# Optimization experiments

Hardware: AMD Instinct MI355X
Metric: run time of the kernel (lower is better)

## Reference

```python
import jax, jax.numpy as jnp
import numpy as np

V, D, H, HD, L, T, B = 65, 384, 6, 64, 6, 256, 64
EPS = 1e-3  # keras LayerNormalization default epsilon


def setup_inputs() -> dict:
    key = jax.random.key(0)
    ks = jax.random.split(key, 12)
    s = 0.02
    n = lambda k, shp: jax.random.normal(k, shp, dtype=jnp.float32) * s
    return {
        "idx": jax.random.randint(ks[0], (B, T), 0, V),
        "tok_emb": n(ks[1], (V, D)),
        "pos_emb": n(ks[2], (T, D)),
        "Wq": n(ks[3], (L, H, D, HD)),
        "Wk": n(ks[4], (L, H, D, HD)),
        "Wv": n(ks[5], (L, H, D, HD)),
        "Wproj": n(ks[6], (L, D, D)),
        "bproj": jnp.zeros((L, D), jnp.float32),
        "W1": n(ks[7], (L, D, 4 * D)),
        "b1": jnp.zeros((L, 4 * D), jnp.float32),
        "W2": n(ks[8], (L, 4 * D, D)),
        "b2": jnp.zeros((L, D), jnp.float32),
        "ln1_g": jnp.ones((L, D), jnp.float32),
        "ln1_b": jnp.zeros((L, D), jnp.float32),
        "ln2_g": jnp.ones((L, D), jnp.float32),
        "ln2_b": jnp.zeros((L, D), jnp.float32),
        "lnf_g": jnp.ones((D,), jnp.float32),
        "lnf_b": jnp.zeros((D,), jnp.float32),
        "Whead": n(ks[9], (D, V)),
        "bhead": jnp.zeros((V,), jnp.float32),
    }


def _ln(x, g, b):
    m = jnp.mean(x, axis=-1, keepdims=True)
    v = jnp.mean(jnp.square(x - m), axis=-1, keepdims=True)
    return (x - m) * jax.lax.rsqrt(v + EPS) * g + b


def reference(idx, tok_emb, pos_emb, Wq, Wk, Wv, Wproj, bproj, W1, b1, W2, b2,
              ln1_g, ln1_b, ln2_g, ln2_b, lnf_g, lnf_b, Whead, bhead):
    Bn, Tn = idx.shape
    x = tok_emb[idx] + pos_emb[:Tn]  # [B,T,D]
    mask = jnp.tril(jnp.ones((Tn, Tn), dtype=bool))
    scale = jnp.float32(D) ** -0.5  # NOTE: original scales by full C=n_embd, not head_size
    for l in range(L):
        h = _ln(x, ln1_g[l], ln1_b[l])
        q = jnp.einsum('btd,hdk->bhtk', h, Wq[l])
        k = jnp.einsum('btd,hdk->bhtk', h, Wk[l])
        v = jnp.einsum('btd,hdk->bhtk', h, Wv[l])
        wei = jnp.einsum('bhtk,bhsk->bhts', q, k) * scale
        wei = jnp.where(mask, wei, -jnp.inf)
        wei = jax.nn.softmax(wei, axis=-1)
        att = jnp.einsum('bhts,bhsk->bhtk', wei, v)
        att = att.transpose(0, 2, 1, 3).reshape(Bn, Tn, D)  # concat heads
        x = x + att @ Wproj[l] + bproj[l]
        h2 = _ln(x, ln2_g[l], ln2_b[l])
        x = x + jax.nn.relu(h2 @ W1[l] + b1[l]) @ W2[l] + b2[l]
    x = _ln(x, lnf_g, lnf_b)
    return x @ Whead + bhead  # logits [B,T,V]
```

## Files before the change

### kernel.cpp

```cpp
#include <hip/hip_runtime.h>
#include <hip/hip_bf16.h>

#define B_  64
#define T_  256
#define D_  384
#define H_  6
#define HD_ 64
#define L_  6
#define V_  65
#define BT  (B_*T_)

typedef __hip_bfloat16 bf16;
typedef unsigned short u16;
typedef short s16;
typedef __attribute__((ext_vector_type(8))) short bf16x8;
typedef __attribute__((ext_vector_type(4))) float f32x4;

#define OFF_QKV   0
#define OFF_PROJ  442368
#define OFF_W1T   589824
#define OFF_W2T   1179648
#define OFF_BPROJ 1769472
#define OFF_B1    1769856
#define OFF_B2    1771392
#define OFF_LN1G  1771776
#define OFF_LN1B  1772160
#define OFF_LN2G  1772544
#define OFF_LN2B  1772928
#define WBUF_E    1773312
#define HOFF_WHT  0
#define HOFF_BH   24960
#define HOFF_LNFG 25088
#define HOFF_LNFB 25472
#define HBUF_E    25856

__device__ __forceinline__ float u2f(u16 u) {
  union { unsigned i; float f; } c; c.i = ((unsigned)u) << 16; return c.f;
}
__device__ __forceinline__ bf16 f2b(float x) { return __float2bfloat16(x); }
__device__ __forceinline__ float b2f(bf16 x) { return __bfloat162float(x); }
__device__ __forceinline__ u16 f2u(float x) { bf16 h = f2b(x); return *(u16*)&h; }

__device__ __forceinline__ float pload(const void* p, size_t i, bool f32w) {
  return f32w ? ((const float*)p)[i] : u2f(((const u16*)p)[i]);
}

__device__ __forceinline__ void swz(int gid, int ntc, int mtiles,
                                    int& nt, int& mblk) {
  if ((mtiles & 7) == 0) {
    int per = ntc << 3;
    int g   = gid / per;
    int rem = gid - g * per;
    nt   = rem >> 3;
    mblk = (g << 3) + (rem & 7);
  } else {
    nt   = gid / mtiles;
    mblk = gid - nt * mtiles;
  }
}

__global__ __launch_bounds__(256) void detect_kernel(
    const void* p1,  const void* p2,  const void* p3,  const void* p4,
    const void* p5,  const void* p6,  const void* p7,  const void* p8,
    const void* p9,  const void* p10, const void* p11, const void* p12,
    const void* p13, const void* p14, const void* p15, const void* p16,
    const void* p17, const void* p18, const void* p19,
    const int* __restrict__ idx, unsigned* flags)
{
  const void* ps[20] = {nullptr, p1, p2, p3, p4, p5, p6, p7, p8, p9, p10,
                        p11, p12, p13, p14, p15, p16, p17, p18, p19};
  const int esz[20] = {16384, 24960, 98304, 884736, 884736, 884736, 884736,
                       2304, 3538944, 9216, 3538944, 2304, 2304, 2304, 2304,
                       2304, 384, 384, 24960, 65};
  __shared__ int r1[256], r2[256];
  int bid = blockIdx.x, tid = threadIdx.x;
  if (bid == 19) {
    int z = 0;
    for (int m = tid; m < 4096; m += 256) z += (idx[2 * m + 1] == 0) ? 1 : 0;
    r1[tid] = z; __syncthreads();
    for (int s = 128; s > 0; s >>= 1) {
      if (tid < s) r1[tid] += r1[tid + s];
      __syncthreads();
    }
    if (tid == 0) flags[20] = (r1[0] >= 4000) ? 1u : 0u;
    return;
  }
  int j = bid + 1;
  const u16* p = (const u16*)ps[j];
  int ns = esz[j] / 2; if (ns > 1024) ns = 1024;
  int band = 0, nz = 0;
  for (int i = tid; i < ns; i += 256) {
    u16 lo = p[2 * i], hi = p[2 * i + 1];
    int e = (lo >> 7) & 0xFF;
    band += (e >= 100 && e <= 127) ? 1 : 0;
    nz   += (lo | hi) ? 1 : 0;
  }
  r1[tid] = band; r2[tid] = nz; __syncthreads();
  for (int s = 128; s > 0; s >>= 1) {
    if (tid < s) { r1[tid] += r1[tid + s]; r2[tid] += r2[tid + s]; }
    __syncthreads();
  }
  if (tid == 0) flags[j] = (r2[0] > 0 && r1[0] * 2 < ns) ? 1u : 0u;
}

__global__ void const_kernel(float* out, int n, float val) {
  int i = blockIdx.x * 256 + threadIdx.x;
  if (i < n) out[i] = val;
}

__device__ __forceinline__ float conv_val(int e, int l,
    const void* Wq, const void* Wk, const void* Wv, const void* Wproj,
    const void* bproj, const void* W1, const void* b1, const void* W2,
    const void* b2, const void* ln1g, const void* ln1b, const void* ln2g,
    const void* ln2b, const unsigned* __restrict__ flags)
{
  float v;
  if (e < OFF_PROJ) {
    int math = e / 24576;
    int rem  = e - math * 24576;
    int hd = rem / 384, d = rem - hd * 384;
    int mat = math / 6, hh = math - mat * 6;
    const void* src = (mat == 0 ? Wq : mat == 1 ? Wk : Wv);
    v = pload(src, ((size_t)(l * 6 + hh) * 384 + d) * 64 + hd, flags[3 + mat] != 0);
  } else if (e < OFF_W1T) {
    int e2 = e - OFF_PROJ;
    int n = e2 / 384, d = e2 - n * 384;
    v = pload(Wproj, ((size_t)l * 384 + d) * 384 + n, flags[6] != 0);
  } else if (e < OFF_W2T) {
    int e2 = e - OFF_W1T;
    int n = e2 / 384, d = e2 - n * 384;
    v = pload(W1, ((size_t)l * 384 + d) * 1536 + n, flags[8] != 0);
  } else if (e < OFF_BPROJ) {
    int e2 = e - OFF_W2T;
    int n = e2 / 1536, k = e2 - n * 1536;
    v = pload(W2, ((size_t)l * 1536 + k) * 384 + n, flags[10] != 0);
  } else {
    int e2 = e - OFF_BPROJ;
    if      (e2 < 384)  v = pload(bproj, (size_t)l * 384 + e2, flags[7] != 0);
    else if (e2 < 1920) v = pload(b1, (size_t)l * 1536 + (e2 - 384), flags[9] != 0);
    else if (e2 < 2304) v = pload(b2, (size_t)l * 384 + (e2 - 1920), flags[11] != 0);
    else if (e2 < 2688) v = pload(ln1g, (size_t)l * 384 + (e2 - 2304), flags[12] != 0);
    else if (e2 < 3072) v = pload(ln1b, (size_t)l * 384 + (e2 - 2688), flags[13] != 0);
    else if (e2 < 3456) v = pload(ln2g, (size_t)l * 384 + (e2 - 3072), flags[14] != 0);
    else                v = pload(ln2b, (size_t)l * 384 + (e2 - 3456), flags[15] != 0);
  }
  return v;
}

__global__ __launch_bounds__(256) void conv_layer(
    const void* Wq, const void* Wk, const void* Wv, const void* Wproj,
    const void* bproj, const void* W1, const void* b1, const void* W2,
    const void* b2, const void* ln1g, const void* ln1b, const void* ln2g,
    const void* ln2b, const unsigned* __restrict__ flags,
    bf16* __restrict__ dst, int l)
{
  int e = blockIdx.x * 256 + threadIdx.x;
  if (e >= WBUF_E) return;
  dst[e] = f2b(conv_val(e, l, Wq, Wk, Wv, Wproj, bproj, W1, b1, W2, b2,
                        ln1g, ln1b, ln2g, ln2b, flags));
}

__global__ __launch_bounds__(256) void convT(
    const void* Wq, const void* Wk, const void* Wv, const void* Wproj,
    const void* W1, const void* W2,
    const unsigned* __restrict__ flags, bf16* __restrict__ dst)
{
  __shared__ float lds[64][65];
  int g = blockIdx.x;
  int l = g / 432, t = g - l * 432;
  const void* sp; bool f32w;
  size_t s_base; int s_rstride;
  size_t d_base; int d_rstride;
  if (t < 108) {
    int mh = t / 6, dt = t - mh * 6;
    int mat = mh / 6;
    sp = (mat == 0 ? Wq : mat == 1 ? Wk : Wv);
    f32w = flags[3 + mat] != 0;
    s_base = ((size_t)l * 6 * 384 + (size_t)(mh - mat * 6) * 384 + dt * 64) * 64;
    s_rstride = 64;
    d_base = (size_t)OFF_QKV + (size_t)mh * 24576 + dt * 64;
    d_rstride = 384;
  } else if (t < 144) {
    int u = t - 108; int nt = u / 6, dt = u - nt * 6;
    sp = Wproj; f32w = flags[6] != 0;
    s_base = ((size_t)l * 384 + dt * 64) * 384 + nt * 64;
    s_rstride = 384;
    d_base = (size_t)OFF_PROJ + (size_t)nt * 64 * 384 + dt * 64;
    d_rstride = 384;
  } else if (t < 288) {
    int u = t - 144; int nt = u / 6, dt = u - nt * 6;
    sp = W1; f32w = flags[8] != 0;
    s_base = ((size_t)l * 384 + dt * 64) * 1536 + nt * 64;
    s_rstride = 1536;
    d_base = (size_t)OFF_W1T + (size_t)nt * 64 * 384 + dt * 64;
    d_rstride = 384;
  } else {
    int u = t - 288; int kt = u / 6, nt = u - kt * 6;
    sp = W2; f32w = flags[10] != 0;
    s_base = ((size_t)l * 1536 + kt * 64) * 384 + nt * 64;
    s_rstride = 384;
    d_base = (size_t)OFF_W2T + (size_t)nt * 64 * 1536 + kt * 64;
    d_rstride = 1536;
  }
  int tid = threadIdx.x;
  int rq = tid >> 6, c = tid & 63;
#pragma unroll
  for (int p = 0; p < 16; p++) {
    int r = p * 4 + rq;
    lds[c][r] = pload(sp, s_base + (size_t)r * s_rstride + c, f32w);
  }
  __syncthreads();
  bf16* dp = dst + (size_t)l * WBUF_E + d_base;
#pragma unroll
  for (int p = 0; p < 16; p++) {
    int cc = p * 4 + rq;
    dp[(size_t)cc * d_rstride + c] = f2b(lds[cc][c]);
  }
}

__global__ __launch_bounds__(256) void convsmall(
    const void* Wq, const void* Wk, const void* Wv, const void* Wproj,
    const void* bproj, const void* W1, const void* b1, const void* W2,
    const void* b2, const void* ln1g, const void* ln1b, const void* ln2g,
    const void* ln2b, const unsigned* __restrict__ flags,
    bf16* __restrict__ dst)
{
  int g = blockIdx.x * 256 + threadIdx.x;
  if (g >= 6 * (WBUF_E - OFF_BPROJ)) return;
  int l = g / (WBUF_E - OFF_BPROJ);
  int e = OFF_BPROJ + (g - l * (WBUF_E - OFF_BPROJ));
  dst[(size_t)l * WBUF_E + e] =
      f2b(conv_val(e, l, Wq, Wk, Wv, Wproj, bproj, W1, b1, W2, b2,
                   ln1g, ln1b, ln2g, ln2b, flags));
}

__global__ __launch_bounds__(256) void conv_head(
    const void* Wh, const void* bh, const void* lnfg, const void* lnfb,
    const unsigned* __restrict__ flags, bf16* __restrict__ dst)
{
  int e = blockIdx.x * 256 + threadIdx.x;
  if (e >= HBUF_E) return;
  float v = 0.f;
  if (e < HOFF_BH) {
    int n = e / 384, d = e - n * 384;
    v = pload(Wh, (size_t)d * 65 + n, flags[18] != 0);
  } else if (e < 25025) {
    v = pload(bh, e - HOFF_BH, flags[19] != 0);
  } else if (e < HOFF_LNFG) {
    v = 0.f;
  } else if (e < HOFF_LNFB) {
    v = pload(lnfg, e - HOFF_LNFG, flags[16] != 0);
  } else {
    v = pload(lnfb, e - HOFF_LNFB, flags[17] != 0);
  }
  dst[e] = f2b(v);
}

__global__ __launch_bounds__(256) void embed_kernel(
    const void* __restrict__ idx, const void* __restrict__ tok,
    const void* __restrict__ pos, bf16* __restrict__ x,
    const unsigned* __restrict__ flags)
{
  int i   = blockIdx.x * 256 + threadIdx.x;
  int tkn = i / D_;
  int d   = i - tkn * D_;
  int t   = tkn & (T_ - 1);
  long long tix;
  if (flags[20]) tix = ((const long long*)idx)[tkn];
  else           tix = ((const int*)idx)[tkn];
  float v = pload(tok, (size_t)tix * D_ + d, flags[1] != 0)
          + pload(pos, (size_t)t * D_ + d, flags[2] != 0);
  x[i] = f2b(v);
}

__global__ __launch_bounds__(256) void lnw_kernel(
    const bf16* __restrict__ x, const u16* __restrict__ g,
    const u16* __restrict__ b, bf16* __restrict__ hc, int tok0)
{
  int w = threadIdx.x >> 6, lane = threadIdx.x & 63;
  int lm = blockIdx.x * 4 + w;
  const u16* xr = (const u16*)x + (size_t)(tok0 + lm) * D_;
  float v[6]; float s = 0.f;
#pragma unroll
  for (int j = 0; j < 3; j++) {
    unsigned pk = *(const unsigned*)(xr + 2 * lane + 128 * j);
    v[2 * j]     = u2f((u16)(pk & 0xFFFF));
    v[2 * j + 1] = u2f((u16)(pk >> 16));
    s += v[2 * j] + v[2 * j + 1];
  }
#pragma unroll
  for (int o = 1; o < 64; o <<= 1) s += __shfl_xor(s, o, 64);
  float mean = s * (1.0f / D_);
  float sq = 0.f;
#pragma unroll
  for (int j = 0; j < 6; j++) { float d0 = v[j] - mean; sq += d0 * d0; }
#pragma unroll
  for (int o = 1; o < 64; o <<= 1) sq += __shfl_xor(sq, o, 64);
  float inv = 1.0f / sqrtf(sq * (1.0f / D_) + 1e-3f);
  u16* hr = (u16*)hc + (size_t)lm * D_;
#pragma unroll
  for (int j = 0; j < 3; j++) {
    int d = 2 * lane + 128 * j;
    unsigned gg = *(const unsigned*)(g + d);
    unsigned bb = *(const unsigned*)(b + d);
    u16 o0 = f2u((v[2 * j]     - mean) * inv * u2f((u16)(gg & 0xFFFF)) + u2f((u16)(bb & 0xFFFF)));
    u16 o1 = f2u((v[2 * j + 1] - mean) * inv * u2f((u16)(gg >> 16))    + u2f((u16)(bb >> 16)));
    *(unsigned*)(hr + d) = ((unsigned)o1 << 16) | o0;
  }
}

__device__ __forceinline__ void gll16(const void* g, void* l) {
  __builtin_amdgcn_global_load_lds(
      (const __attribute__((address_space(1))) unsigned*)g,
      (__attribute__((address_space(3))) unsigned*)l, 16, 0, 0);
}

__device__ __forceinline__ bf16x8 ldfrag(const s16* lds, int r, int s) {
  return *(const bf16x8*)(lds + r * 64 + ((s ^ (r & 7)) << 3));
}

template<int NT, class Epi>
__device__ __forceinline__ void mcore(
    s16* __restrict__ As, s16* __restrict__ Wl,
    const u16* __restrict__ A, const u16* __restrict__ WT,
    int N, int K, int arow0, int n0, Epi epi)
{
  constexpr int MREP = (NT == 128) ? 4 : 2;
  constexpr int WPW  = NT / 32;
  int tid = threadIdx.x;
  int w = tid >> 6, lane = tid & 63;
  int quad = lane >> 4, l15 = lane & 15;
  int r8 = lane >> 3;
  int sl = ((lane & 7) ^ r8) * 8;
  int wm = (NT == 128) ? ((w >> 1) * 64) : (w * 32);
  int wn = (NT == 128) ? ((w & 1) * 64) : 0;

  f32x4 acc[MREP][4];
#pragma unroll
  for (int i = 0; i < MREP; i++)
#pragma unroll
    for (int j = 0; j < 4; j++) acc[i][j] = (f32x4){0.f, 0.f, 0.f, 0.f};

  const u16* Ag[4];
#pragma unroll
  for (int i = 0; i < 4; i++)
    Ag[i] = A + (size_t)(arow0 + (w * 4 + i) * 8 + r8) * K + sl;
  const u16* Wg[WPW];
#pragma unroll
  for (int i = 0; i < WPW; i++)
    Wg[i] = WT + (size_t)(n0 + (w * WPW + i) * 8 + r8) * K + sl;

  for (int k0 = 0; k0 < K; k0 += 64) {
    __syncthreads();
#pragma unroll
    for (int i = 0; i < 4; i++)
      gll16(Ag[i] + k0, As + (w * 4 + i) * 512);
#pragma unroll
    for (int i = 0; i < WPW; i++)
      gll16(Wg[i] + k0, Wl + (w * WPW + i) * 512);
    __syncthreads();
#pragma unroll
    for (int kh = 0; kh < 2; kh++) {
      bf16x8 am[MREP], bn[4];
#pragma unroll
      for (int i = 0; i < MREP; i++)
        am[i] = ldfrag(As, wm + i * 16 + l15, kh * 4 + quad);
#pragma unroll
      for (int j = 0; j < 4; j++)
        bn[j] = ldfrag(Wl, wn + j * 16 + l15, kh * 4 + quad);
#pragma unroll
      for (int i = 0; i < MREP; i++)
#pragma unroll
        for (int j = 0; j < 4; j++)
          acc[i][j] = __builtin_amdgcn_mfma_f32_16x16x32_bf16(am[i], bn[j], acc[i][j], 0, 0, 0);
    }
  }

#pragma unroll
  for (int i = 0; i < MREP; i++)
#pragma unroll
    for (int j = 0; j < 4; j++)
#pragma unroll
      for (int r = 0; r < 4; r++) {
        int m = wm + i * 16 + quad * 4 + r;
        int n = n0 + wn + j * 16 + l15;
        if (n < N) epi(m, n, acc[i][j][r]);
      }
}

template<class EpiV, class EpiR>
__device__ __forceinline__ void mcoreB(
    s16* __restrict__ SM,
    const u16* __restrict__ A, const u16* __restrict__ WT,
    int K, int arow0, int n0, EpiV epiv, EpiR epir)
{
  s16* As = SM;
  s16* Wl = SM + 128 * 64;
  int tid = threadIdx.x;
  int w = tid >> 6, lane = tid & 63;
  int quad = lane >> 4, l15 = lane & 15;
  int r8 = lane >> 3;
  int sl = ((lane & 7) ^ r8) * 8;
  int wm = (w >> 1) * 64, wn = (w & 1) * 64;

  f32x4 acc[4][4];
#pragma unroll
  for (int i = 0; i < 4; i++)
#pragma unroll
    for (int j = 0; j < 4; j++) acc[i][j] = (f32x4){0.f, 0.f, 0.f, 0.f};

  const u16* Ag[4];
#pragma unroll
  for (int i = 0; i < 4; i++)
    Ag[i] = A + (size_t)(arow0 + (w * 4 + i) * 8 + r8) * K + sl;
  const u16* Wg[4];
#pragma unroll
  for (int i = 0; i < 4; i++)
    Wg[i] = WT + (size_t)(n0 + (w * 4 + i) * 8 + r8) * K + sl;

  for (int k0 = 0; k0 < K; k0 += 64) {
    __syncthreads();
#pragma unroll
    for (int i = 0; i < 4; i++)
      gll16(Ag[i] + k0, As + (w * 4 + i) * 512);
#pragma unroll
    for (int i = 0; i < 4; i++)
      gll16(Wg[i] + k0, Wl + (w * 4 + i) * 512);
    __syncthreads();
#pragma unroll
    for (int kh = 0; kh < 2; kh++) {
      bf16x8 am[4], bn[4];
#pragma unroll
      for (int i = 0; i < 4; i++)
        am[i] = ldfrag(As, wm + i * 16 + l15, kh * 4 + quad);
#pragma unroll
      for (int j = 0; j < 4; j++)
        bn[j] = ldfrag(Wl, wn + j * 16 + l15, kh * 4 + quad);
#pragma unroll
      for (int i = 0; i < 4; i++)
#pragma unroll
        for (int j = 0; j < 4; j++)
          acc[i][j] = __builtin_amdgcn_mfma_f32_16x16x32_bf16(am[i], bn[j], acc[i][j], 0, 0, 0);
    }
  }

  __syncthreads();
#pragma unroll
  for (int i = 0; i < 4; i++)
#pragma unroll
    for (int j = 0; j < 4; j++)
#pragma unroll
      for (int r = 0; r < 4; r++) {
        int m = wm + i * 16 + quad * 4 + r;
        int nloc = wn + j * 16 + l15;
        int nl6 = nloc & 63;
        SM[((nloc >> 6) << 13) + m * 64 +
           ((((nl6 >> 3) ^ (m & 7)) << 3)) + (nl6 & 7)] = epiv(nloc, acc[i][j][r]);
      }
  __syncthreads();
  int row = tid >> 1, hf = tid & 1;
  const s16* src = SM + (hf << 13) + row * 64;
#pragma unroll
  for (int c = 0; c < 8; c++) {
    bf16x8 v8 = *(const bf16x8*)(src + ((c ^ (row & 7)) << 3));
    epir(row, hf, c, v8);
  }
}

__global__ __launch_bounds__(256) void qkv128(
    const bf16* hc, const bf16* Wbuf, bf16* qkvc, int MCa, int mtiles)
{
  __shared__ __attribute__((aligned(16))) s16 SM[2 * 128 * 64];
  int nt, mblk;
  swz(blockIdx.x, 9, mtiles, nt, mblk);
  int n0 = nt * 128, mloc0 = mblk * 128;
  auto epiv = [&](int nloc, float v) -> s16 { return (s16)f2u(v); };
  auto epir = [&](int row, int hf, int c, bf16x8 v8) {
    int nn = n0 + hf * 64;
    int mat = nn / 384;
    int hh = (nn - mat * 384) >> 6;
    *(bf16x8*)((u16*)qkvc + (size_t)mat * MCa * D_ + (size_t)hh * MCa * HD_
               + (size_t)(mloc0 + row) * HD_ + c * 8) = v8;
  };
  mcoreB(SM, (const u16*)hc, (const u16*)Wbuf + OFF_QKV,
         D_, mloc0, n0, epiv, epir);
}

__global__ __launch_bounds__(256) void ffn1_128(
    const bf16* hc, const bf16* Wbuf, bf16* midc, int mtiles)
{
  __shared__ __attribute__((aligned(16))) s16 SM[2 * 128 * 64];
  int nt, mblk;
  swz(blockIdx.x, 12, mtiles, nt, mblk);
  int n0 = nt * 128, m0 = mblk * 128;
  const bf16* bias = (const bf16*)Wbuf + OFF_B1;
  auto epiv = [&](int nloc, float v) -> s16 {
    float r = v + b2f(bias[n0 + nloc]);
    return (s16)f2u(fmaxf(r, 0.f));
  };
  auto epir = [&](int row, int hf, int c, bf16x8 v8) {
    *(bf16x8*)((u16*)midc + (size_t)(m0 + row) * (4 * D_)
               + n0 + hf * 64 + c * 8) = v8;
  };
  mcoreB(SM, (const u16*)hc, (const u16*)Wbuf + OFF_W1T,
         D_, m0, n0, epiv, epir);
}

__global__ __launch_bounds__(256) void proj_mfma(
    const bf16* A, const bf16* Wbuf, bf16* x, int tok0, int mtiles)
{
  __shared__ __attribute__((aligned(16))) s16 As[128 * 64];
  __shared__ __attribute__((aligned(16))) s16 Ws[64 * 64];
  int nt, mblk;
  swz(blockIdx.x, 6, mtiles, nt, mblk);
  int n0 = nt * 64, m0 = mblk * 128;
  const bf16* bias = (const bf16*)Wbuf + OFF_BPROJ;
  auto epi = [&](int m, int n, float v) {
    size_t o = (size_t)(tok0 + m0 + m) * D_ + n;
    x[o] = f2b(v + b2f(bias[n]) + b2f(x[o]));
  };
  mcore<64>(As, Ws, (const u16*)A,
            (const u16*)Wbuf + OFF_PROJ, D_, D_, m0, n0, epi);
}

__global__ __launch_bounds__(256) void ffn2_mfma(
    const bf16* midc, const bf16* Wbuf, bf16* x, int tok0, int mtiles)
{
  __shared__ __attribute__((aligned(16))) s16 As[128 * 64];
  __shared__ __attribute__((aligned(16))) s16 Ws[64 * 64];
  int nt, mblk;
  swz(blockIdx.x, 6, mtiles, nt, mblk);
  int n0 = nt * 64, m0 = mblk * 128;
  const bf16* bias = (const bf16*)Wbuf + OFF_B2;
  auto epi = [&](int m, int n, float v) {
    size_t o = (size_t)(tok0 + m0 + m) * D_ + n;
    x[o] = f2b(v + b2f(bias[n]) + b2f(x[o]));
  };
  mcore<64>(As, Ws, (const u16*)midc,
            (const u16*)Wbuf + OFF_W2T, D_, 4 * D_, m0, n0, epi);
}

__global__ __launch_bounds__(256) void head_mfma(
    const bf16* hc, const bf16* Hbuf, float* out, int tok0)
{
  __shared__ __attribute__((aligned(16))) s16 As[128 * 64];
  __shared__ __attribute__((aligned(16))) s16 Ws[64 * 64];
  int n0 = blockIdx.x * 64, m0 = blockIdx.y * 128;
  const bf16* bias = (const bf16*)Hbuf + HOFF_BH;
  auto epi = [&](int m, int n, float v) {
    out[(size_t)(tok0 + m0 + m) * V_ + n] = v + b2f(bias[n]);
  };
  mcore<64>(As, Ws, (const u16*)hc,
            (const u16*)Hbuf + HOFF_WHT, V_, D_, m0, n0, epi);
}

__global__ __launch_bounds__(256) void attn4_kernel(
    const bf16* __restrict__ Q, const bf16* __restrict__ K,
    const bf16* __restrict__ V, bf16* __restrict__ att, int MCa)
{
  __shared__ s16 Qs[64 * 72];
  __shared__ s16 Ks[64 * 72];
  __shared__ __attribute__((aligned(16))) s16 Vt[64 * 64];
  __shared__ s16 Ps[4][16 * 72];
  const float scale = 0.05103103630798288f;
  int tid = threadIdx.x;
  int w = tid >> 6, lane = tid & 63;
  int quad = lane >> 4, l15 = lane & 15;
  int bid = blockIdx.x;
  int qt = bid & 3;
  int bh = bid >> 2;
  int b = bh / H_, h = bh - b * H_;
  size_t base = ((size_t)h * MCa + (size_t)b * T_) * HD_;
  int q0 = qt * 64;
  int cq = qt;

  int rstg = (tid & 7) + 8 * (tid >> 6);
  int sstg = (tid >> 3) & 7;

#pragma unroll
  for (int i = 0; i < 2; i++) {
    int r = rstg + 32 * i;
    *(bf16x8*)&Qs[r * 72 + sstg * 8] =
        *(const bf16x8*)((const u16*)Q + base + (size_t)(q0 + r) * HD_ + sstg * 8);
  }

  float mrow[4] = {-1e30f, -1e30f, -1e30f, -1e30f};
  float lrow[4] = {0.f, 0.f, 0.f, 0.f};
  f32x4 O[4];
#pragma unroll
  for (int nt = 0; nt < 4; nt++) O[nt] = (f32x4){0.f, 0.f, 0.f, 0.f};

  for (int c = 0; c <= cq; c++) {
    __syncthreads();
#pragma unroll
    for (int i = 0; i < 2; i++) {
      int r = rstg + 32 * i;
      *(bf16x8*)&Ks[r * 72 + sstg * 8] =
          *(const bf16x8*)((const u16*)K + base + (size_t)(c * 64 + r) * HD_ + sstg * 8);
      bf16x8 vv =
          *(const bf16x8*)((const u16*)V + base + (size_t)(c * 64 + r) * HD_ + sstg * 8);
      int rs = r >> 3, rl = r & 7;
      int so = ((rs ^ sstg) << 3) + rl;
#pragma unroll
      for (int k = 0; k < 8; k++)
        Vt[(sstg * 8 + k) * 64 + so] = vv[k];
    }
    __syncthreads();

    f32x4 S[4];
#pragma unroll
    for (int nt = 0; nt < 4; nt++) S[nt] = (f32x4){0.f, 0.f, 0.f, 0.f};
#pragma unroll
    for (int ks = 0; ks < 2; ks++) {
      int kk = ks * 32 + quad * 8;
      bf16x8 a = *(const bf16x8*)&Qs[(w * 16 + l15) * 72 + kk];
#pragma unroll
      for (int nt = 0; nt < 4; nt++) {
        bf16x8 bb8 = *(const bf16x8*)&Ks[(nt * 16 + l15) * 72 + kk];
        S[nt] = __builtin_amdgcn_mfma_f32_16x16x32_bf16(a, bb8, S[nt], 0, 0, 0);
      }
    }

#pragma unroll
    for (int nt = 0; nt < 4; nt++)
#pragma unroll
      for (int r = 0; r < 4; r++) {
        int qrow = q0 + w * 16 + quad * 4 + r;
        int sg = c * 64 + nt * 16 + l15;
        float v = S[nt][r] * scale;
        S[nt][r] = (sg <= qrow) ? v : -1e30f;
      }

    float alpha[4];
#pragma unroll
    for (int r = 0; r < 4; r++) {
      float mc = fmaxf(fmaxf(S[0][r], S[1][r]), fmaxf(S[2][r], S[3][r]));
#pragma unroll
      for (int o = 1; o < 16; o <<= 1) mc = fmaxf(mc, __shfl_xor(mc, o, 64));
      float mn = fmaxf(mrow[r], mc);
      alpha[r] = __expf(mrow[r] - mn);
      mrow[r] = mn;
      float s = 0.f;
#pragma unroll
      for (int nt = 0; nt < 4; nt++) {
        float p = __expf(S[nt][r] - mn);
        S[nt][r] = p;
        s += p;
      }
#pragma unroll
      for (int o = 1; o < 16; o <<= 1) s += __shfl_xor(s, o, 64);
      lrow[r] = lrow[r] * alpha[r] + s;
    }
#pragma unroll
    for (int nt = 0; nt < 4; nt++)
#pragma unroll
      for (int r = 0; r < 4; r++) O[nt][r] *= alpha[r];

#pragma unroll
    for (int nt = 0; nt < 4; nt++)
#pragma unroll
      for (int r = 0; r < 4; r++)
        Ps[w][(quad * 4 + r) * 72 + nt * 16 + l15] = (s16)f2u(S[nt][r]);
    __syncthreads();
#pragma unroll
    for (int ks = 0; ks < 2; ks++) {
      bf16x8 a = *(const bf16x8*)&Ps[w][l15 * 72 + ks * 32 + quad * 8];
#pragma unroll
      for (int nt = 0; nt < 4; nt++) {
        int d = nt * 16 + l15;
        bf16x8 bb8 = *(const bf16x8*)&Vt[d * 64 +
            (((ks * 4 + quad) ^ ((d >> 3) & 7)) << 3)];
        O[nt] = __builtin_amdgcn_mfma_f32_16x16x32_bf16(a, bb8, O[nt], 0, 0, 0);
      }
    }
  }

#pragma unroll
  for (int r = 0; r < 4; r++) {
    float invl = 1.0f / lrow[r];
#pragma unroll
    for (int nt = 0; nt < 4; nt++) {
      int qrow = q0 + w * 16 + quad * 4 + r;
      att[(size_t)(b * T_ + qrow) * D_ + h * HD_ + nt * 16 + l15] =
          f2b(O[nt][r] * invl);
    }
  }
}

extern "C" void kernel_launch(void* const* d_in, const int* in_sizes, int n_in,
                              void* d_out, int out_size, void* d_ws, size_t ws_size,
                              hipStream_t stream)
{
  float* out = (float*)d_out;
  dim3 blk(256);
  int outg = (out_size + 255) / 256;

  static const int expected[20] = {
      16384, 24960, 98304, 884736, 884736, 884736, 884736, 2304,
      3538944, 9216, 3538944, 2304, 2304, 2304, 2304, 2304, 384, 384,
      24960, 65};
  if (n_in != 20) { const_kernel<<<outg, blk, 0, stream>>>(out, out_size, 5.0f); return; }
  for (int i = 0; i < 20; i++)
    if (in_sizes[i] != expected[i]) {
      const_kernel<<<outg, blk, 0, stream>>>(out, out_size, 10.0f * (i + 1));
      return;
    }
  if (out_size != BT * V_) { const_kernel<<<outg, blk, 0, stream>>>(out, out_size, 7.0f); return; }

  const void* idx   = d_in[0];
  const void* tok   = d_in[1];
  const void* pos   = d_in[2];
  const void* Wq    = d_in[3];
  const void* Wk    = d_in[4];
  const void* Wv    = d_in[5];
  const void* Wproj = d_in[6];
  const void* bproj = d_in[7];
  const void* W1    = d_in[8];
  const void* b1    = d_in[9];
  const void* W2    = d_in[10];
  const void* b2    = d_in[11];
  const void* ln1g  = d_in[12];
  const void* ln1b  = d_in[13];
  const void* ln2g  = d_in[14];
  const void* ln2b  = d_in[15];
  const void* lnfg  = d_in[16];
  const void* lnfb  = d_in[17];
  const void* Whead = d_in[18];
  const void* bhead = d_in[19];

  const size_t off_x  = 256;
  const size_t off_wb = off_x + (size_t)BT * D_ * 2;
  int nl = 6;
  size_t off_hb = off_wb + (size_t)nl * WBUF_E * 2;
  size_t fixed  = off_hb + ((size_t)HBUF_E * 2 + 63) / 64 * 64;
  size_t minchunk = (size_t)5 * (BT / 64) * D_ * 2;
  if (ws_size < fixed + minchunk) {
    nl = 1;
    off_hb = off_wb + (size_t)WBUF_E * 2;
    fixed  = off_hb + ((size_t)HBUF_E * 2 + 63) / 64 * 64;
  }
  if (ws_size < fixed) {
    const_kernel<<<outg, blk, 0, stream>>>(out, out_size, 0.0f);
    return;
  }
  size_t region = ws_size - fixed;

  int nc = 0;
  const int candn[7] = {1, 2, 4, 8, 16, 32, 64};
  for (int i = 0; i < 7; i++)
    if ((size_t)5 * (BT / candn[i]) * D_ * 2 <= region) { nc = candn[i]; break; }
  if (!nc) { const_kernel<<<outg, blk, 0, stream>>>(out, out_size, 0.0f); return; }
  const int MCc = BT / nc;
  const int CBc = MCc / T_;
  const int mtiles = MCc / 128;

  char* wsb = (char*)d_ws;
  unsigned* flags = (unsigned*)wsb;
  bf16*   x    = (bf16*)(wsb + off_x);
  bf16*   Wbuf = (bf16*)(wsb + off_wb);
  bf16*   Hbuf = (bf16*)(wsb + off_hb);
  bf16*   hc   = (bf16*)(wsb + fixed);
  bf16*   qkvc = hc + (size_t)MCc * D_;
  bf16*   attc = qkvc + (size_t)3 * MCc * D_;
  bf16*   midc = qkvc;

  detect_kernel<<<dim3(20), blk, 0, stream>>>(
      tok, pos, Wq, Wk, Wv, Wproj, bproj, W1, b1, W2, b2,
      ln1g, ln1b, ln2g, ln2b, lnfg, lnfb, Whead, bhead,
      (const int*)idx, flags);
  embed_kernel<<<dim3(BT * D_ / 256), blk, 0, stream>>>(idx, tok, pos, x, flags);
  conv_head<<<dim3((HBUF_E + 255) / 256), blk, 0, stream>>>(
      Whead, bhead, lnfg, lnfb, flags, Hbuf);
  if (nl == 6) {
    convT<<<dim3(6 * 432), blk, 0, stream>>>(
        Wq, Wk, Wv, Wproj, W1, W2, flags, Wbuf);
    convsmall<<<dim3((6 * (WBUF_E - OFF_BPROJ) + 255) / 256), blk, 0, stream>>>(
        Wq, Wk, Wv, Wproj, bproj, W1, b1, W2, b2,
        ln1g, ln1b, ln2g, ln2b, flags, Wbuf);
  }

  for (int l = 0; l < L_; l++) {
    const bf16* Wl = Wbuf + (nl == 6 ? (size_t)l * WBUF_E : 0);
    if (nl == 1)
      conv_layer<<<dim3((WBUF_E + 255) / 256), blk, 0, stream>>>(
          Wq, Wk, Wv, Wproj, bproj, W1, b1, W2, b2,
          ln1g, ln1b, ln2g, ln2b, flags, Wbuf, l);
    for (int c = 0; c < nc; c++) {
      int tok0 = c * MCc;
      lnw_kernel<<<dim3(MCc / 4), blk, 0, stream>>>(
          x, (const u16*)Wl + OFF_LN1G, (const u16*)Wl + OFF_LN1B, hc, tok0);
      qkv128<<<dim3(9 * mtiles), blk, 0, stream>>>(hc, Wl, qkvc, MCc, mtiles);
      attn4_kernel<<<dim3(CBc * H_ * 4), blk, 0, stream>>>(
          qkvc, qkvc + (size_t)MCc * D_, qkvc + (size_t)2 * MCc * D_, attc, MCc);
      proj_mfma<<<dim3(6 * mtiles), blk, 0, stream>>>(attc, Wl, x, tok0, mtiles);
    }
    for (int f = 0; f < nc; f++) {
      int tok0 = f * MCc;
      lnw_kernel<<<dim3(MCc / 4), blk, 0, stream>>>(
          x, (const u16*)Wl + OFF_LN2G, (const u16*)Wl + OFF_LN2B, hc, tok0);
      ffn1_128<<<dim3(12 * mtiles), blk, 0, stream>>>(hc, Wl, midc, mtiles);
      ffn2_mfma<<<dim3(6 * mtiles), blk, 0, stream>>>(midc, Wl, x, tok0, mtiles);
    }
  }

  for (int c = 0; c < nc; c++) {
    int tok0 = c * MCc;
    lnw_kernel<<<dim3(MCc / 4), blk, 0, stream>>>(
        x, (const u16*)Hbuf + HOFF_LNFG, (const u16*)Hbuf + HOFF_LNFB, hc, tok0);
    head_mfma<<<dim3(2, MCc / 128), blk, 0, stream>>>(hc, Hbuf, out, tok0);
  }
}
```

Measured before the change: 1.124 ms.

## Use direct global-to-LDS loads and staged vectorized epilogue for proj/ffn2 GEMMs

Adds a new 128x64 MFMA GEMM core that loads A and W tiles straight into LDS with 16-byte global-to-LDS transfers, and uses it for the projection and FFN2 kernels. The epilogue now stages fp32 accumulators through swizzled shared memory, so each thread reads back 8 contiguous outputs and does vectorized 16-byte residual reads, bias adds and writes. This replaces scattered per-element residual updates. It increases shared memory per block and adds extra barriers and an LDS round trip in the epilogue.

```diff
diff --git a/kernel.cpp b/kernel.cpp
--- a/kernel.cpp
+++ b/kernel.cpp
@@ -467,6 +467,88 @@
   }
 }
 
+template<class Fin>
+__device__ __forceinline__ void mcoreB64(
+    s16* __restrict__ SM,
+    const u16* __restrict__ A, const u16* __restrict__ WT,
+    int K, int arow0, int n0, Fin fin)
+{
+  s16* As = SM;
+  s16* Wl = SM + 128 * 64;
+  int tid = threadIdx.x;
+  int w = tid >> 6, lane = tid & 63;
+  int quad = lane >> 4, l15 = lane & 15;
+  int r8 = lane >> 3;
+  int sl = ((lane & 7) ^ r8) * 8;
+  int wm = w * 32;
+
+  f32x4 acc[2][4];
+#pragma unroll
+  for (int i = 0; i < 2; i++)
+#pragma unroll
+    for (int j = 0; j < 4; j++) acc[i][j] = (f32x4){0.f, 0.f, 0.f, 0.f};
+
+  const u16* Ag[4];
+#pragma unroll
+  for (int i = 0; i < 4; i++)
+    Ag[i] = A + (size_t)(arow0 + (w * 4 + i) * 8 + r8) * K + sl;
+  const u16* Wg[2];
+#pragma unroll
+  for (int i = 0; i < 2; i++)
+    Wg[i] = WT + (size_t)(n0 + (w * 2 + i) * 8 + r8) * K + sl;
+
+  for (int k0 = 0; k0 < K; k0 += 64) {
+    __syncthreads();
+#pragma unroll
+    for (int i = 0; i < 4; i++)
+      gll16(Ag[i] + k0, As + (w * 4 + i) * 512);
+#pragma unroll
+    for (int i = 0; i < 2; i++)
+      gll16(Wg[i] + k0, Wl + (w * 2 + i) * 512);
+    __syncthreads();
+#pragma unroll
+    for (int kh = 0; kh < 2; kh++) {
+      bf16x8 am[2], bn[4];
+#pragma unroll
+      for (int i = 0; i < 2; i++)
+        am[i] = ldfrag(As, wm + i * 16 + l15, kh * 4 + quad);
+#pragma unroll
+      for (int j = 0; j < 4; j++)
+        bn[j] = ldfrag(Wl, j * 16 + l15, kh * 4 + quad);
+#pragma unroll
+      for (int i = 0; i < 2; i++)
+#pragma unroll
+        for (int j = 0; j < 4; j++)
+          acc[i][j] = __builtin_amdgcn_mfma_f32_16x16x32_bf16(am[i], bn[j], acc[i][j], 0, 0, 0);
+    }
+  }
+
+  __syncthreads();
+  float* SMf = (float*)SM;
+#pragma unroll
+  for (int i = 0; i < 2; i++)
+#pragma unroll
+    for (int j = 0; j < 4; j++)
+#pragma unroll
+      for (int r = 0; r < 4; r++) {
+        int m = wm + i * 16 + quad * 4 + r;
+        int n = j * 16 + l15;
+        SMf[m * 64 + (n ^ ((m & 7) << 2))] = acc[i][j][r];
+      }
+  __syncthreads();
+  int row = tid >> 1, hf = tid & 1;
+  int mask = (row & 7) << 2;
+  const float* rp = SMf + row * 64;
+#pragma unroll
+  for (int c8 = 0; c8 < 4; c8++) {
+    int cb = hf * 32 + c8 * 8;
+    float v[8];
+    *(f32x4*)(v)     = *(const f32x4*)(rp + ((cb)     ^ mask));
+    *(f32x4*)(v + 4) = *(const f32x4*)(rp + ((cb + 4) ^ mask));
+    fin(row, cb, v);
+  }
+}
+
 __global__ __launch_bounds__(256) void qkv128(
     const bf16* hc, const bf16* Wbuf, bf16* qkvc, int MCa, int mtiles)
 {
@@ -509,35 +591,47 @@
 __global__ __launch_bounds__(256) void proj_mfma(
     const bf16* A, const bf16* Wbuf, bf16* x, int tok0, int mtiles)
 {
-  __shared__ __attribute__((aligned(16))) s16 As[128 * 64];
-  __shared__ __attribute__((aligned(16))) s16 Ws[64 * 64];
+  __shared__ __attribute__((aligned(16))) s16 SM[2 * 128 * 64];
   int nt, mblk;
   swz(blockIdx.x, 6, mtiles, nt, mblk);
   int n0 = nt * 64, m0 = mblk * 128;
-  const bf16* bias = (const bf16*)Wbuf + OFF_BPROJ;
-  auto epi = [&](int m, int n, float v) {
-    size_t o = (size_t)(tok0 + m0 + m) * D_ + n;
-    x[o] = f2b(v + b2f(bias[n]) + b2f(x[o]));
+  const u16* bias = (const u16*)Wbuf + OFF_BPROJ;
+  auto fin = [&](int row, int cb, const float* v) {
+    size_t o = (size_t)(tok0 + m0 + row) * D_ + n0 + cb;
+    u16* xp = (u16*)x + o;
+    bf16x8 xr = *(const bf16x8*)xp;
+    bf16x8 bb = *(const bf16x8*)(bias + n0 + cb);
+    bf16x8 ov;
+#pragma unroll
+    for (int k = 0; k < 8; k++)
+      ov[k] = (s16)f2u(v[k] + u2f((u16)bb[k]) + u2f((u16)xr[k]));
+    *(bf16x8*)xp = ov;
   };
-  mcore<64>(As, Ws, (const u16*)A,
-            (const u16*)Wbuf + OFF_PROJ, D_, D_, m0, n0, epi);
+  mcoreB64(SM, (const u16*)A, (const u16*)Wbuf + OFF_PROJ,
+           D_, m0, n0, fin);
 }
 
 __global__ __launch_bounds__(256) void ffn2_mfma(
     const bf16* midc, const bf16* Wbuf, bf16* x, int tok0, int mtiles)
 {
-  __shared__ __attribute__((aligned(16))) s16 As[128 * 64];
-  __shared__ __attribute__((aligned(16))) s16 Ws[64 * 64];
+  __shared__ __attribute__((aligned(16))) s16 SM[2 * 128 * 64];
   int nt, mblk;
   swz(blockIdx.x, 6, mtiles, nt, mblk);
   int n0 = nt * 64, m0 = mblk * 128;
-  const bf16* bias = (const bf16*)Wbuf + OFF_B2;
-  auto epi = [&](int m, int n, float v) {
-    size_t o = (size_t)(tok0 + m0 + m) * D_ + n;
-    x[o] = f2b(v + b2f(bias[n]) + b2f(x[o]));
+  const u16* bias = (const u16*)Wbuf + OFF_B2;
+  auto fin = [&](int row, int cb, const float* v) {
+    size_t o = (size_t)(tok0 + m0 + row) * D_ + n0 + cb;
+    u16* xp = (u16*)x + o;
+    bf16x8 xr = *(const bf16x8*)xp;
+    bf16x8 bb = *(const bf16x8*)(bias + n0 + cb);
+    bf16x8 ov;
+#pragma unroll
+    for (int k = 0; k < 8; k++)
+      ov[k] = (s16)f2u(v[k] + u2f((u16)bb[k]) + u2f((u16)xr[k]));
+    *(bf16x8*)xp = ov;
   };
-  mcore<64>(As, Ws, (const u16*)midc,
-            (const u16*)Wbuf + OFF_W2T, D_, 4 * D_, m0, n0, epi);
+  mcoreB64(SM, (const u16*)midc, (const u16*)Wbuf + OFF_W2T,
+           4 * D_, m0, n0, fin);
 }
 
 __global__ __launch_bounds__(256) void head_mfma(
```

After: 1.126 ms. Within noise of the previous version (+0.2%).
